# Kernel optimization log

Measured on AMD Instinct MI355X. Metric: run time of the kernel, lower is better.

The kernel has to match this reference:

```python
import jax, jax.numpy as jnp
import numpy as np

SCALE = 1.0 / 4.0      # alpha / dim
MULTIPLIER = 1.0

def _act(h):
    return jax.nn.gelu(h, approximate=False)  # torch nn.GELU(approximate='none')

def setup_inputs() -> dict:
    key = jax.random.key(0)
    ks = jax.random.split(key, 9)
    B, T, D = 64, 77, 768
    N, R = 1024, 4
    return {
        "x":     jax.random.normal(ks[0], (B, T, D), jnp.float32),
        "W_org": jax.random.normal(ks[1], (D, D), jnp.float32) * 0.02,
        "b_org": jax.random.normal(ks[2], (D,), jnp.float32) * 0.02,
        "w1":    jax.random.normal(ks[3], (N, D, R), jnp.float32) * 0.02,
        "b1":    jax.random.normal(ks[4], (N, R), jnp.float32) * 0.02,
        "mid_w": jax.random.normal(ks[5], (N, R, R), jnp.float32) * 0.02,
        "mid_b": jax.random.normal(ks[6], (N, R), jnp.float32) * 0.02,
        "w_out": jax.random.normal(ks[7], (N, R, D), jnp.float32) * 0.02,
        "b_out": jax.random.normal(ks[8], (N, D), jnp.float32) * 0.02,
    }

def reference(x, W_org, b_org, w1, b1, mid_w, mid_b, w_out, b_out):
    # per-concept low-rank MLP: h in [B, T, N, R]
    h = jnp.einsum('btd,ndh->btnh', x, w1) + b1[None, None]
    h = _act(h)
    # repeated 'h' in 'nhh' takes the diagonal of mid_w (elementwise scale),
    # exactly matching torch.einsum semantics in the source.
    h = jnp.einsum('btnh,nhh->btnh', h, mid_w) + mid_b[None, None]
    h = _act(h)
    # fuse out-projection with sum over concepts: sum_n (h_n @ w_out_n) + sum_n b_out_n
    up = jnp.einsum('btnh,nhd->btd', h, w_out) + jnp.sum(b_out, axis=0)
    org = x @ W_org.T + b_org
    return org + up * (MULTIPLIER * SCALE)
```

## Files before the change

kernel.cpp:

```cpp
#include <hip/hip_runtime.h>
#include <hip/hip_bf16.h>

#define M_TOK 4928
#define M_PAD 5120
#define D_DIM 768
#define NR    4096
#define K_CAT 4864
#define KT_ALL 152

typedef __bf16 bf16;
typedef unsigned char u8;
typedef __attribute__((ext_vector_type(8))) __bf16 bf16x8;
typedef __attribute__((ext_vector_type(4))) float f32x4;
typedef __attribute__((address_space(1))) uint32_t gu32;
typedef __attribute__((address_space(3))) uint32_t su32;

#define GLDS(P, LDSP) \
  __builtin_amdgcn_global_load_lds((gu32*)(P), (su32*)(LDSP), 16, 0, 0)

__device__ __forceinline__ uint32_t pk_fp8x4(float a, float b, float c, float d) {
  uint32_t w = 0;
  w = (uint32_t)__builtin_amdgcn_cvt_pk_fp8_f32(a, b, (int)w, false);
  w = (uint32_t)__builtin_amdgcn_cvt_pk_fp8_f32(c, d, (int)w, true);
  return w;
}

__device__ __forceinline__ float act_fast(float v) {
  float e = __builtin_amdgcn_exp2f(v * -2.4554677f);
  return v * __builtin_amdgcn_rcpf(1.0f + e);
}

__device__ __forceinline__ int xcd_swizzle(int orig, int nwg) {
  const int q = nwg >> 3, r = nwg & 7;
  const int x = orig & 7, rest = orig >> 3;
  return (x < r ? x * (q + 1) : r * (q + 1) + (x - r) * q) + rest;
}


__global__ __launch_bounds__(256) void k_prep_x(const float* __restrict__ x,
                                                bf16* __restrict__ Xb) {
  int idx = (blockIdx.x * 256 + threadIdx.x) * 4;
  if (idx >= M_PAD * D_DIM) return;
  int m = idx / D_DIM;
  union { uint2 u; bf16 h[4]; } o;
  if (m < M_TOK) {
    float4 v = *(const float4*)(x + idx);
    o.h[0] = (bf16)v.x; o.h[1] = (bf16)v.y; o.h[2] = (bf16)v.z; o.h[3] = (bf16)v.w;
  } else {
    o.h[0] = o.h[1] = o.h[2] = o.h[3] = (bf16)0.0f;
  }
  *(uint2*)(Xb + idx) = o.u;
}

__global__ __launch_bounds__(256) void k_prep_xq(const float* __restrict__ x,
                                                 u8* __restrict__ Xq) {
  int idx = (blockIdx.x * 256 + threadIdx.x) * 4;
  if (idx >= M_PAD * D_DIM) return;
  int m = idx / D_DIM;
  uint32_t w = 0;
  if (m < M_TOK) {
    float4 v = *(const float4*)(x + idx);
    w = pk_fp8x4(v.x, v.y, v.z, v.w);
  }
  *(uint32_t*)(Xq + idx) = w;
}

__global__ __launch_bounds__(256) void k_prep_w1q(const float* __restrict__ w1,
                                                  u8* __restrict__ W1q) {
  int gid = blockIdx.x * 256 + threadIdx.x;
  int n = gid / 96, oct = gid % 96;
  const float4* src = (const float4*)w1 + (size_t)n * D_DIM + oct * 8;
  float e[4][8];
#pragma unroll
  for (int d = 0; d < 8; ++d) {
    float4 v = src[d];
    e[0][d] = v.x * 64.0f; e[1][d] = v.y * 64.0f;
    e[2][d] = v.z * 64.0f; e[3][d] = v.w * 64.0f;
  }
  size_t base = (size_t)n * 4 * D_DIM + oct * 8;
#pragma unroll
  for (int r = 0; r < 4; ++r) {
    uint2 o;
    o.x = pk_fp8x4(e[r][0], e[r][1], e[r][2], e[r][3]);
    o.y = pk_fp8x4(e[r][4], e[r][5], e[r][6], e[r][7]);
    *(uint2*)(W1q + base + (size_t)r * D_DIM) = o;
  }
}

__global__ __launch_bounds__(256) void k_prep_w2t_t(const float* __restrict__ w_out,
                                                    bf16* __restrict__ W2t) {
  __shared__ float S[64 * 65];
  const int bk = blockIdx.x & 63, bd = blockIdx.x >> 6;
  const int k0 = bk * 64, d0 = bd * 64;
  const int tr = threadIdx.x >> 4;
  const int tc = (threadIdx.x & 15) * 4;
#pragma unroll
  for (int p = 0; p < 4; ++p) {
    const int kr = tr + p * 16;
    float4 v = *(const float4*)(w_out + (size_t)(k0 + kr) * D_DIM + d0 + tc);
    S[kr * 65 + tc + 0] = v.x; S[kr * 65 + tc + 1] = v.y;
    S[kr * 65 + tc + 2] = v.z; S[kr * 65 + tc + 3] = v.w;
  }
  __syncthreads();
#pragma unroll
  for (int p = 0; p < 4; ++p) {
    const int dr = tr + p * 16;
    union { uint2 u; bf16 h[4]; } o;
#pragma unroll
    for (int i = 0; i < 4; ++i) o.h[i] = (bf16)(0.25f * S[(tc + i) * 65 + dr]);
    *(uint2*)(W2t + (size_t)(d0 + dr) * K_CAT + k0 + tc) = o.u;
  }
}

__global__ __launch_bounds__(256) void k_prep_w2t_org(const float* __restrict__ W_org,
                                                      bf16* __restrict__ W2t) {
  int idx = (blockIdx.x * 256 + threadIdx.x) * 4;
  if (idx >= D_DIM * D_DIM) return;
  int d = idx / D_DIM, c = idx % D_DIM;
  float4 v = *(const float4*)(W_org + idx);
  union { uint2 u; bf16 h[4]; } o;
  o.h[0] = (bf16)v.x; o.h[1] = (bf16)v.y; o.h[2] = (bf16)v.z; o.h[3] = (bf16)v.w;
  *(uint2*)(W2t + (size_t)d * K_CAT + NR + c) = o.u;
}

__global__ __launch_bounds__(256) void k_bias_partial(const float* __restrict__ b_out,
                                                      float* __restrict__ partial) {
  int b = blockIdx.x;
  for (int d = threadIdx.x; d < D_DIM; d += 256) {
    float s = 0.0f;
    for (int n = b * 32; n < b * 32 + 32; ++n) s += b_out[n * D_DIM + d];
    partial[b * D_DIM + d] = s;
  }
}

__global__ __launch_bounds__(256) void k_bias_final2(const float* __restrict__ partial,
                                                     const float* __restrict__ b_org,
                                                     const float* __restrict__ mid_w,
                                                     float* __restrict__ bias_total,
                                                     float* __restrict__ diag) {
  int b = blockIdx.x;
  if (b < 3) {
    int d = b * 256 + threadIdx.x;
    if (d >= D_DIM) return;
    float s = 0.0f;
#pragma unroll
    for (int p = 0; p < 32; ++p) s += partial[p * D_DIM + d];
    bias_total[d] = b_org[d] + 0.25f * s;
  } else {
    int j = (b - 3) * 256 + threadIdx.x;
    diag[j] = mid_w[(j >> 2) * 16 + (j & 3) * 5];
  }
}


__device__ __forceinline__ int swz_slot(int kg, int lr) {
  return (kg ^ ((lr >> 1) & 3)) << 3;
}

__device__ __forceinline__ void stage_unit8(const bf16* g, int ld, int row0, int col0,
                                            bf16* lds) {
  const int lane = threadIdx.x & 63;
  const int wave = threadIdx.x >> 6;
  const int src_slot = (lane & 3) ^ ((lane >> 3) & 3);
#pragma unroll
  for (int c = 0; c < 2; ++c) {
    const int chunk = wave * 2 + c;
    const int row = row0 + chunk * 16 + (lane >> 2);
    const bf16* gp = g + (size_t)row * ld + col0 + (src_slot << 3);
    GLDS(gp, lds + chunk * 512);
  }
}


#define G1F_IT(S_, DO_STG, LAST_)                                               \
  {                                                                             \
    if (LAST_) { asm volatile("s_waitcnt vmcnt(0)" ::: "memory"); }             \
    else       { asm volatile("s_waitcnt vmcnt(4)" ::: "memory"); }             \
    asm volatile("s_barrier" ::: "memory");                                     \
    long a0[4], a1[4], b0[4], b1[4];                                            \
    _Pragma("unroll") for (int i = 0; i < 4; ++i) {                             \
      a0[i] = *(const long*)(&As[S_][aOff + i * 1024]);                         \
      a1[i] = *(const long*)(&As[S_][(aOff ^ 32) + i * 1024]);                  \
    }                                                                           \
    _Pragma("unroll") for (int j = 0; j < 4; ++j) {                             \
      b0[j] = *(const long*)(&Bs[S_][bOff + j * 1024]);                         \
      b1[j] = *(const long*)(&Bs[S_][(bOff ^ 32) + j * 1024]);                  \
    }                                                                           \
    if (DO_STG) {                                                               \
      GLDS(aP0, &As[((S_) + 2) % 3][ldsC0]);                                    \
      GLDS(aP1, &As[((S_) + 2) % 3][ldsC1]);                                    \
      GLDS(bP0, &Bs[((S_) + 2) % 3][ldsC0]);                                    \
      GLDS(bP1, &Bs[((S_) + 2) % 3][ldsC1]);                                    \
      aP0 += 64; aP1 += 64; bP0 += 64; bP1 += 64;                               \
    }                                                                           \
    _Pragma("unroll") for (int i = 0; i < 4; ++i)                               \
      _Pragma("unroll") for (int j = 0; j < 4; ++j)                             \
        acc[i][j] = __builtin_amdgcn_mfma_f32_16x16x32_fp8_fp8(b0[j], a0[i], acc[i][j], 0, 0, 0); \
    _Pragma("unroll") for (int i = 0; i < 4; ++i)                               \
      _Pragma("unroll") for (int j = 0; j < 4; ++j)                             \
        acc[i][j] = __builtin_amdgcn_mfma_f32_16x16x32_fp8_fp8(b1[j], a1[i], acc[i][j], 0, 0, 0); \
  }

__global__ __launch_bounds__(256) void k_gemm1(const u8* __restrict__ Xq,
                                               const u8* __restrict__ W1q,
                                               bf16* __restrict__ H2,
                                               const float* __restrict__ b1,
                                               const float* __restrict__ diag,
                                               const float* __restrict__ midb) {
  __shared__ u8 As[3][128 * 64];
  __shared__ u8 Bs[3][128 * 64];
  const int wgid = xcd_swizzle(blockIdx.x, 39 * 32);
  const int bmt = wgid >> 5;
  const int bnt = wgid & 31;
  const int m0 = bmt * 128, n0 = bnt * 128;
  const int lane = threadIdx.x & 63;
  const int wave = threadIdx.x >> 6;
  const int wm = wave >> 1, wn = wave & 1;
  const int lr = lane & 15, kg = lane >> 4;
  const int slotB = (((kg >> 1) ^ ((lr >> 1) & 3)) << 4) + ((kg & 1) << 3);
  const int aOff = (wm * 64 + lr) * 64 + slotB;
  const int bOff = (wn * 64 + lr) * 64 + slotB;

  const int src_slot = (lane & 3) ^ ((lane >> 3) & 3);
  const int srow = (wave * 2) * 16 + (lane >> 2);
  const u8* aP0 = Xq  + (size_t)(m0 + srow) * D_DIM + (src_slot << 4);
  const u8* aP1 = aP0 + 16 * D_DIM;
  const u8* bP0 = W1q + (size_t)(n0 + srow) * D_DIM + (src_slot << 4);
  const u8* bP1 = bP0 + 16 * D_DIM;
  const int ldsC0 = (wave * 2) * 1024, ldsC1 = ldsC0 + 1024;

  f32x4 acc[4][4];
#pragma unroll
  for (int i = 0; i < 4; ++i)
#pragma unroll
    for (int j = 0; j < 4; ++j) acc[i][j] = (f32x4)(0.0f);

  GLDS(aP0, &As[0][ldsC0]); GLDS(aP1, &As[0][ldsC1]);
  GLDS(bP0, &Bs[0][ldsC0]); GLDS(bP1, &Bs[0][ldsC1]);
  aP0 += 64; aP1 += 64; bP0 += 64; bP1 += 64;
  GLDS(aP0, &As[1][ldsC0]); GLDS(aP1, &As[1][ldsC1]);
  GLDS(bP0, &Bs[1][ldsC0]); GLDS(bP1, &Bs[1][ldsC1]);
  aP0 += 64; aP1 += 64; bP0 += 64; bP1 += 64;

  for (int g = 0; g < 3; ++g) {
    G1F_IT(0, true, false)
    G1F_IT(1, true, false)
    G1F_IT(2, true, false)
  }
  G1F_IT(0, true, false)
  G1F_IT(1, false, false)
  G1F_IT(2, false, true)

#pragma unroll
  for (int j = 0; j < 4; ++j) {
    const int jcb = n0 + wn * 64 + j * 16 + kg * 4;
    const float4 b1v = *(const float4*)(b1 + jcb);
    const float4 dgv = *(const float4*)(diag + jcb);
    const float4 mbv = *(const float4*)(midb + jcb);
#pragma unroll
    for (int i = 0; i < 4; ++i) {
      const int mr = m0 + wm * 64 + i * 16 + lr;
      union { uint2 u; bf16 h[4]; } o;
      float h;
      h = act_fast(fmaf(acc[i][j][0], 0.015625f, b1v.x)); o.h[0] = (bf16)act_fast(h * dgv.x + mbv.x);
      h = act_fast(fmaf(acc[i][j][1], 0.015625f, b1v.y)); o.h[1] = (bf16)act_fast(h * dgv.y + mbv.y);
      h = act_fast(fmaf(acc[i][j][2], 0.015625f, b1v.z)); o.h[2] = (bf16)act_fast(h * dgv.z + mbv.z);
      h = act_fast(fmaf(acc[i][j][3], 0.015625f, b1v.w)); o.h[3] = (bf16)act_fast(h * dgv.w + mbv.w);
      *(uint2*)(H2 + (size_t)mr * NR + jcb) = o.u;
    }
  }
}


#define ENGINE(KT0, KT1, STAGE_A, STAGE_B)                                      \
  {                                                                             \
    STAGE_A((KT0) + 0, 0); STAGE_B((KT0) + 0, 0);                               \
    STAGE_A((KT0) + 1, 1); STAGE_B((KT0) + 1, 1);                               \
    STAGE_A((KT0) + 2, 2); STAGE_B((KT0) + 2, 2);                               \
    asm volatile("s_waitcnt vmcnt(8)" ::: "memory");                            \
    asm volatile("s_barrier" ::: "memory");                                     \
    for (int t = (KT0); t < (KT1); ++t) {                                       \
      const int s  = (t - (KT0)) & 3;                                           \
      const int st = (t - (KT0) + 3) & 3;                                       \
      const bool more = (t + 3 < (KT1));                                        \
      bf16x8 a[8], b[4];                                                        \
      _Pragma("unroll") for (int i = 0; i < 4; ++i)                             \
        a[i] = *(const bf16x8*)(As[s] + aBase + i * 512);                       \
      _Pragma("unroll") for (int j = 0; j < 4; ++j)                             \
        b[j] = *(const bf16x8*)(Bs[s] + bBase + j * 512);                       \
      if (more) { STAGE_A(t + 3, st); }                                         \
      asm volatile("s_barrier" ::: "memory");                                   \
      __builtin_amdgcn_s_setprio(1);                                            \
      _Pragma("unroll") for (int i = 0; i < 4; ++i)                             \
        _Pragma("unroll") for (int j = 0; j < 4; ++j)                           \
          acc[i][j] = __builtin_amdgcn_mfma_f32_16x16x32_bf16(b[j], a[i], acc[i][j], 0, 0, 0); \
      __builtin_amdgcn_s_setprio(0);                                            \
      asm volatile("s_barrier" ::: "memory");                                   \
      _Pragma("unroll") for (int i = 0; i < 4; ++i)                             \
        a[4 + i] = *(const bf16x8*)(As[s] + aBase + 2048 + i * 512);            \
      if (more) { STAGE_B(t + 3, st); }                                         \
      {                                                                         \
        int ahead = ((KT1) - 1) - (t + 1);                                      \
        if (ahead >= 2)      { asm volatile("s_waitcnt vmcnt(8)" ::: "memory"); } \
        else if (ahead == 1) { asm volatile("s_waitcnt vmcnt(4)" ::: "memory"); } \
        else                 { asm volatile("s_waitcnt vmcnt(0)" ::: "memory"); } \
      }                                                                         \
      asm volatile("s_barrier" ::: "memory");                                   \
      __builtin_amdgcn_s_setprio(1);                                            \
      _Pragma("unroll") for (int i = 0; i < 4; ++i)                             \
        _Pragma("unroll") for (int j = 0; j < 4; ++j)                           \
          acc[4 + i][j] = __builtin_amdgcn_mfma_f32_16x16x32_bf16(b[j], a[4 + i], acc[4 + i][j], 0, 0, 0); \
      __builtin_amdgcn_s_setprio(0);                                            \
      asm volatile("s_barrier" ::: "memory");                                   \
    }                                                                           \
  }

template <int SPLITS>
__global__ __launch_bounds__(512) void k_gemm2(const bf16* __restrict__ H2,
                                               const bf16* __restrict__ Xb,
                                               const bf16* __restrict__ W2t,
                                               void* __restrict__ outp,
                                               const float* __restrict__ bias) {
  __shared__ bf16 As[4][8192];
  __shared__ bf16 Bs[4][8192];
  const int nwg = 20 * 3 * SPLITS;
  const int wgid = xcd_swizzle(blockIdx.x, nwg);
  const int bmt = wgid / (3 * SPLITS);
  const int rem = wgid % (3 * SPLITS);
  const int ks  = rem / 3;
  const int bnt = rem % 3;
  const int m0 = bmt * 256, n0 = bnt * 256;
  const int lane = threadIdx.x & 63;
  const int wave = threadIdx.x >> 6;
  const int wm = wave >> 2, wn = wave & 3;
  const int lr = lane & 15, kg = lane >> 4;
  const int slotE = swz_slot(kg, lr);
  const int aBase = (wm * 128 + lr) * 32 + slotE;
  const int bBase = (wn * 64 + lr) * 32 + slotE;
  constexpr int KT_PER = KT_ALL / SPLITS;
  const int kt0 = ks * KT_PER, kt1 = kt0 + KT_PER;

  f32x4 acc[8][4];
#pragma unroll
  for (int i = 0; i < 8; ++i)
#pragma unroll
    for (int j = 0; j < 4; ++j) acc[i][j] = (f32x4)(0.0f);

#define G2_SA(kt, buf)                                                  \
  {                                                                     \
    const int k0s = (kt) * 32;                                          \
    if (k0s < NR) stage_unit8(H2, NR, m0, k0s, As[(buf)]);              \
    else          stage_unit8(Xb, D_DIM, m0, k0s - NR, As[(buf)]);      \
  }
#define G2_SB(kt, buf) stage_unit8(W2t, K_CAT, n0, (kt) * 32, Bs[(buf)])
  ENGINE(kt0, kt1, G2_SA, G2_SB)
#undef G2_SA
#undef G2_SB

  if (SPLITS > 1) {
    bf16* dst = (bf16*)outp + (size_t)ks * M_TOK * D_DIM;
#pragma unroll
    for (int j = 0; j < 4; ++j) {
      const int cb = n0 + wn * 64 + j * 16 + kg * 4;
#pragma unroll
      for (int i = 0; i < 8; ++i) {
        const int mr = m0 + wm * 128 + i * 16 + lr;
        if (mr < M_TOK) {
          union { uint2 u; bf16 h[4]; } o;
          o.h[0] = (bf16)acc[i][j][0]; o.h[1] = (bf16)acc[i][j][1];
          o.h[2] = (bf16)acc[i][j][2]; o.h[3] = (bf16)acc[i][j][3];
          *(uint2*)(dst + (size_t)mr * D_DIM + cb) = o.u;
        }
      }
    }
  } else {
    float* dst = (float*)outp;
#pragma unroll
    for (int j = 0; j < 4; ++j) {
      const int cb = n0 + wn * 64 + j * 16 + kg * 4;
      const f32x4 bv = *(const f32x4*)(bias + cb);
#pragma unroll
      for (int i = 0; i < 8; ++i) {
        const int mr = m0 + wm * 128 + i * 16 + lr;
        if (mr < M_TOK) {
          f32x4 o = acc[i][j] + bv;
          *(f32x4*)(dst + (size_t)mr * D_DIM + cb) = o;
        }
      }
    }
  }
}

template <int SPLITS>
__global__ __launch_bounds__(256) void k_reduce(const bf16* __restrict__ padd,
                                                const float* __restrict__ bias,
                                                float* __restrict__ out) {
  int idx = (blockIdx.x * 256 + threadIdx.x) * 4;
  if (idx >= M_TOK * D_DIM) return;
  float4 s = *(const float4*)(bias + (idx % D_DIM));
#pragma unroll
  for (int p = 0; p < SPLITS; ++p) {
    union { uint2 u; bf16 h[4]; } v;
    v.u = *(const uint2*)(padd + (size_t)p * M_TOK * D_DIM + idx);
    s.x += (float)v.h[0]; s.y += (float)v.h[1];
    s.z += (float)v.h[2]; s.w += (float)v.h[3];
  }
  *(float4*)(out + idx) = s;
}


extern "C" void kernel_launch(void* const* d_in, const int* in_sizes, int n_in,
                              void* d_out, int out_size, void* d_ws, size_t ws_size,
                              hipStream_t stream) {
  const float* x     = (const float*)d_in[0];
  const float* W_org = (const float*)d_in[1];
  const float* b_org = (const float*)d_in[2];
  const float* w1    = (const float*)d_in[3];
  const float* b1    = (const float*)d_in[4];
  const float* mid_w = (const float*)d_in[5];
  const float* mid_b = (const float*)d_in[6];
  const float* w_out = (const float*)d_in[7];
  const float* b_out = (const float*)d_in[8];
  float* out = (float*)d_out;

  bf16* Xb   = (bf16*)d_ws;
  bf16* W2t  = Xb  + (size_t)M_PAD * D_DIM;
  bf16* H2   = W2t + (size_t)D_DIM * K_CAT;
  float* bias    = (float*)(H2 + (size_t)M_PAD * NR);
  float* partial = bias + 1024;
  float* diag    = partial + 32 * D_DIM;
  u8*   Xq   = (u8*)(diag + NR);
  u8*   W1q  = Xq + (size_t)M_PAD * D_DIM;
  bf16* padd = (bf16*)(W1q + (size_t)NR * D_DIM);

  const size_t base_bytes = (size_t)((char*)padd - (char*)d_ws);
  const size_t per_split  = (size_t)M_TOK * D_DIM * sizeof(bf16);
  int S = 1;
  if (ws_size >= base_bytes + 4 * per_split)      S = 4;
  else if (ws_size >= base_bytes + 2 * per_split) S = 2;

  k_prep_x      <<<(M_PAD * D_DIM / 4) / 256, 256, 0, stream>>>(x, Xb);
  k_prep_xq     <<<(M_PAD * D_DIM / 4) / 256, 256, 0, stream>>>(x, Xq);
  k_prep_w1q    <<<384, 256, 0, stream>>>(w1, W1q);
  k_prep_w2t_t  <<<64 * 12, 256, 0, stream>>>(w_out, W2t);
  k_prep_w2t_org<<<(D_DIM * D_DIM / 4 + 255) / 256, 256, 0, stream>>>(W_org, W2t);
  k_bias_partial<<<32, 256, 0, stream>>>(b_out, partial);
  k_bias_final2 <<<19, 256, 0, stream>>>(partial, b_org, mid_w, bias, diag);

  k_gemm1<<<39 * 32, 256, 0, stream>>>(Xq, W1q, H2, b1, diag, mid_b);

  const int red_grid = (M_TOK * D_DIM / 4 + 255) / 256;
  if (S == 4) {
    k_gemm2<4><<<20 * 3 * 4, 512, 0, stream>>>(H2, Xb, W2t, padd, bias);
    k_reduce<4><<<red_grid, 256, 0, stream>>>(padd, bias, out);
  } else if (S == 2) {
    k_gemm2<2><<<20 * 3 * 2, 512, 0, stream>>>(H2, Xb, W2t, padd, bias);
    k_reduce<2><<<red_grid, 256, 0, stream>>>(padd, bias, out);
  } else {
    k_gemm2<1><<<20 * 3, 512, 0, stream>>>(H2, Xb, W2t, out, bias);
  }
}
```

Before: 118.9 us.

## Quantize second GEMM to FP8 and split the low-rank and W_org GEMMs

The intermediate activations H2 and the w_out weights are now stored as scaled FP8 instead of bf16. The low-rank out-projection runs as its own fp8 MFMA GEMM with a 4-way K split, using 128x128 tiles and the same pipeline macro as gemm1. The x@W_org part moves to a separate bf16 GEMM that writes bias plus result into out, and the reduce pass then adds the split partials on top. This halves the bytes for the dominant K=4096 operand and doubles MFMA throughput, at the cost of FP8 accuracy loss and an extra kernel launch. The reduce now depends on gemm2b having written out first.

```diff
diff --git a/kernel.cpp b/kernel.cpp
--- a/kernel.cpp
+++ b/kernel.cpp
@@ -3,10 +3,9 @@
 
 #define M_TOK 4928
 #define M_PAD 5120
+#define M_GMM 4992
 #define D_DIM 768
 #define NR    4096
-#define K_CAT 4864
-#define KT_ALL 152
 
 typedef __bf16 bf16;
 typedef unsigned char u8;
@@ -87,8 +86,8 @@
   }
 }
 
-__global__ __launch_bounds__(256) void k_prep_w2t_t(const float* __restrict__ w_out,
-                                                    bf16* __restrict__ W2t) {
+__global__ __launch_bounds__(256) void k_prep_w2q(const float* __restrict__ w_out,
+                                                  u8* __restrict__ W2q) {
   __shared__ float S[64 * 65];
   const int bk = blockIdx.x & 63, bd = blockIdx.x >> 6;
   const int k0 = bk * 64, d0 = bd * 64;
@@ -105,22 +104,20 @@
 #pragma unroll
   for (int p = 0; p < 4; ++p) {
     const int dr = tr + p * 16;
-    union { uint2 u; bf16 h[4]; } o;
-#pragma unroll
-    for (int i = 0; i < 4; ++i) o.h[i] = (bf16)(0.25f * S[(tc + i) * 65 + dr]);
-    *(uint2*)(W2t + (size_t)(d0 + dr) * K_CAT + k0 + tc) = o.u;
-  }
-}
-
-__global__ __launch_bounds__(256) void k_prep_w2t_org(const float* __restrict__ W_org,
-                                                      bf16* __restrict__ W2t) {
+    uint32_t w = pk_fp8x4(16.0f * S[(tc + 0) * 65 + dr], 16.0f * S[(tc + 1) * 65 + dr],
+                          16.0f * S[(tc + 2) * 65 + dr], 16.0f * S[(tc + 3) * 65 + dr]);
+    *(uint32_t*)(W2q + (size_t)(d0 + dr) * NR + k0 + tc) = w;
+  }
+}
+
+__global__ __launch_bounds__(256) void k_prep_worg(const float* __restrict__ W_org,
+                                                   bf16* __restrict__ WorgB) {
   int idx = (blockIdx.x * 256 + threadIdx.x) * 4;
   if (idx >= D_DIM * D_DIM) return;
-  int d = idx / D_DIM, c = idx % D_DIM;
   float4 v = *(const float4*)(W_org + idx);
   union { uint2 u; bf16 h[4]; } o;
   o.h[0] = (bf16)v.x; o.h[1] = (bf16)v.y; o.h[2] = (bf16)v.z; o.h[3] = (bf16)v.w;
-  *(uint2*)(W2t + (size_t)d * K_CAT + NR + c) = o.u;
+  *(uint2*)(WorgB + idx) = o.u;
 }
 
 __global__ __launch_bounds__(256) void k_bias_partial(const float* __restrict__ b_out,
@@ -149,25 +146,6 @@
   } else {
     int j = (b - 3) * 256 + threadIdx.x;
     diag[j] = mid_w[(j >> 2) * 16 + (j & 3) * 5];
-  }
-}
-
-
-__device__ __forceinline__ int swz_slot(int kg, int lr) {
-  return (kg ^ ((lr >> 1) & 3)) << 3;
-}
-
-__device__ __forceinline__ void stage_unit8(const bf16* g, int ld, int row0, int col0,
-                                            bf16* lds) {
-  const int lane = threadIdx.x & 63;
-  const int wave = threadIdx.x >> 6;
-  const int src_slot = (lane & 3) ^ ((lane >> 3) & 3);
-#pragma unroll
-  for (int c = 0; c < 2; ++c) {
-    const int chunk = wave * 2 + c;
-    const int row = row0 + chunk * 16 + (lane >> 2);
-    const bf16* gp = g + (size_t)row * ld + col0 + (src_slot << 3);
-    GLDS(gp, lds + chunk * 512);
   }
 }
 
@@ -203,7 +181,7 @@
 
 __global__ __launch_bounds__(256) void k_gemm1(const u8* __restrict__ Xq,
                                                const u8* __restrict__ W1q,
-                                               bf16* __restrict__ H2,
+                                               u8* __restrict__ H2q,
                                                const float* __restrict__ b1,
                                                const float* __restrict__ diag,
                                                const float* __restrict__ midb) {
@@ -260,146 +238,180 @@
 #pragma unroll
     for (int i = 0; i < 4; ++i) {
       const int mr = m0 + wm * 64 + i * 16 + lr;
-      union { uint2 u; bf16 h[4]; } o;
-      float h;
-      h = act_fast(fmaf(acc[i][j][0], 0.015625f, b1v.x)); o.h[0] = (bf16)act_fast(h * dgv.x + mbv.x);
-      h = act_fast(fmaf(acc[i][j][1], 0.015625f, b1v.y)); o.h[1] = (bf16)act_fast(h * dgv.y + mbv.y);
-      h = act_fast(fmaf(acc[i][j][2], 0.015625f, b1v.z)); o.h[2] = (bf16)act_fast(h * dgv.z + mbv.z);
-      h = act_fast(fmaf(acc[i][j][3], 0.015625f, b1v.w)); o.h[3] = (bf16)act_fast(h * dgv.w + mbv.w);
-      *(uint2*)(H2 + (size_t)mr * NR + jcb) = o.u;
+      float h, f0, f1, f2, f3;
+      h = act_fast(fmaf(acc[i][j][0], 0.015625f, b1v.x)); f0 = act_fast(h * dgv.x + mbv.x);
+      h = act_fast(fmaf(acc[i][j][1], 0.015625f, b1v.y)); f1 = act_fast(h * dgv.y + mbv.y);
+      h = act_fast(fmaf(acc[i][j][2], 0.015625f, b1v.z)); f2 = act_fast(h * dgv.z + mbv.z);
+      h = act_fast(fmaf(acc[i][j][3], 0.015625f, b1v.w)); f3 = act_fast(h * dgv.w + mbv.w);
+      uint32_t w = pk_fp8x4(f0 * 128.0f, f1 * 128.0f, f2 * 128.0f, f3 * 128.0f);
+      *(uint32_t*)(H2q + (size_t)mr * NR + jcb) = w;
     }
   }
 }
 
-
-#define ENGINE(KT0, KT1, STAGE_A, STAGE_B)                                      \
-  {                                                                             \
-    STAGE_A((KT0) + 0, 0); STAGE_B((KT0) + 0, 0);                               \
-    STAGE_A((KT0) + 1, 1); STAGE_B((KT0) + 1, 1);                               \
-    STAGE_A((KT0) + 2, 2); STAGE_B((KT0) + 2, 2);                               \
-    asm volatile("s_waitcnt vmcnt(8)" ::: "memory");                            \
-    asm volatile("s_barrier" ::: "memory");                                     \
-    for (int t = (KT0); t < (KT1); ++t) {                                       \
-      const int s  = (t - (KT0)) & 3;                                           \
-      const int st = (t - (KT0) + 3) & 3;                                       \
-      const bool more = (t + 3 < (KT1));                                        \
-      bf16x8 a[8], b[4];                                                        \
-      _Pragma("unroll") for (int i = 0; i < 4; ++i)                             \
-        a[i] = *(const bf16x8*)(As[s] + aBase + i * 512);                       \
-      _Pragma("unroll") for (int j = 0; j < 4; ++j)                             \
-        b[j] = *(const bf16x8*)(Bs[s] + bBase + j * 512);                       \
-      if (more) { STAGE_A(t + 3, st); }                                         \
-      asm volatile("s_barrier" ::: "memory");                                   \
-      __builtin_amdgcn_s_setprio(1);                                            \
-      _Pragma("unroll") for (int i = 0; i < 4; ++i)                             \
-        _Pragma("unroll") for (int j = 0; j < 4; ++j)                           \
-          acc[i][j] = __builtin_amdgcn_mfma_f32_16x16x32_bf16(b[j], a[i], acc[i][j], 0, 0, 0); \
-      __builtin_amdgcn_s_setprio(0);                                            \
-      asm volatile("s_barrier" ::: "memory");                                   \
-      _Pragma("unroll") for (int i = 0; i < 4; ++i)                             \
-        a[4 + i] = *(const bf16x8*)(As[s] + aBase + 2048 + i * 512);            \
-      if (more) { STAGE_B(t + 3, st); }                                         \
-      {                                                                         \
-        int ahead = ((KT1) - 1) - (t + 1);                                      \
-        if (ahead >= 2)      { asm volatile("s_waitcnt vmcnt(8)" ::: "memory"); } \
-        else if (ahead == 1) { asm volatile("s_waitcnt vmcnt(4)" ::: "memory"); } \
-        else                 { asm volatile("s_waitcnt vmcnt(0)" ::: "memory"); } \
-      }                                                                         \
-      asm volatile("s_barrier" ::: "memory");                                   \
-      __builtin_amdgcn_s_setprio(1);                                            \
-      _Pragma("unroll") for (int i = 0; i < 4; ++i)                             \
-        _Pragma("unroll") for (int j = 0; j < 4; ++j)                           \
-          acc[4 + i][j] = __builtin_amdgcn_mfma_f32_16x16x32_bf16(b[j], a[4 + i], acc[4 + i][j], 0, 0, 0); \
-      __builtin_amdgcn_s_setprio(0);                                            \
-      asm volatile("s_barrier" ::: "memory");                                   \
-    }                                                                           \
-  }
-
-template <int SPLITS>
-__global__ __launch_bounds__(512) void k_gemm2(const bf16* __restrict__ H2,
-                                               const bf16* __restrict__ Xb,
-                                               const bf16* __restrict__ W2t,
-                                               void* __restrict__ outp,
-                                               const float* __restrict__ bias) {
-  __shared__ bf16 As[4][8192];
-  __shared__ bf16 Bs[4][8192];
-  const int nwg = 20 * 3 * SPLITS;
-  const int wgid = xcd_swizzle(blockIdx.x, nwg);
-  const int bmt = wgid / (3 * SPLITS);
-  const int rem = wgid % (3 * SPLITS);
-  const int ks  = rem / 3;
-  const int bnt = rem % 3;
-  const int m0 = bmt * 256, n0 = bnt * 256;
+__global__ __launch_bounds__(256) void k_gemm2a(const u8* __restrict__ H2q,
+                                                const u8* __restrict__ W2q,
+                                                bf16* __restrict__ padd) {
+  __shared__ u8 As[3][128 * 64];
+  __shared__ u8 Bs[3][128 * 64];
+  const int wgid = xcd_swizzle(blockIdx.x, 39 * 6 * 4);
+  const int bmt = wgid / 24;
+  const int rem = wgid % 24;
+  const int ks  = rem / 6;
+  const int bnt = rem % 6;
+  const int m0 = bmt * 128, n0 = bnt * 128;
+  const int kbase = ks * 1024;
   const int lane = threadIdx.x & 63;
   const int wave = threadIdx.x >> 6;
-  const int wm = wave >> 2, wn = wave & 3;
+  const int wm = wave >> 1, wn = wave & 1;
   const int lr = lane & 15, kg = lane >> 4;
-  const int slotE = swz_slot(kg, lr);
-  const int aBase = (wm * 128 + lr) * 32 + slotE;
-  const int bBase = (wn * 64 + lr) * 32 + slotE;
-  constexpr int KT_PER = KT_ALL / SPLITS;
-  const int kt0 = ks * KT_PER, kt1 = kt0 + KT_PER;
-
-  f32x4 acc[8][4];
-#pragma unroll
-  for (int i = 0; i < 8; ++i)
+  const int slotB = (((kg >> 1) ^ ((lr >> 1) & 3)) << 4) + ((kg & 1) << 3);
+  const int aOff = (wm * 64 + lr) * 64 + slotB;
+  const int bOff = (wn * 64 + lr) * 64 + slotB;
+
+  const int src_slot = (lane & 3) ^ ((lane >> 3) & 3);
+  const int srow = (wave * 2) * 16 + (lane >> 2);
+  const u8* aP0 = H2q + (size_t)(m0 + srow) * NR + kbase + (src_slot << 4);
+  const u8* aP1 = aP0 + 16 * NR;
+  const u8* bP0 = W2q + (size_t)(n0 + srow) * NR + kbase + (src_slot << 4);
+  const u8* bP1 = bP0 + 16 * NR;
+  const int ldsC0 = (wave * 2) * 1024, ldsC1 = ldsC0 + 1024;
+
+  f32x4 acc[4][4];
+#pragma unroll
+  for (int i = 0; i < 4; ++i)
 #pragma unroll
     for (int j = 0; j < 4; ++j) acc[i][j] = (f32x4)(0.0f);
 
-#define G2_SA(kt, buf)                                                  \
-  {                                                                     \
-    const int k0s = (kt) * 32;                                          \
-    if (k0s < NR) stage_unit8(H2, NR, m0, k0s, As[(buf)]);              \
-    else          stage_unit8(Xb, D_DIM, m0, k0s - NR, As[(buf)]);      \
-  }
-#define G2_SB(kt, buf) stage_unit8(W2t, K_CAT, n0, (kt) * 32, Bs[(buf)])
-  ENGINE(kt0, kt1, G2_SA, G2_SB)
-#undef G2_SA
-#undef G2_SB
-
-  if (SPLITS > 1) {
-    bf16* dst = (bf16*)outp + (size_t)ks * M_TOK * D_DIM;
-#pragma unroll
-    for (int j = 0; j < 4; ++j) {
-      const int cb = n0 + wn * 64 + j * 16 + kg * 4;
-#pragma unroll
-      for (int i = 0; i < 8; ++i) {
-        const int mr = m0 + wm * 128 + i * 16 + lr;
-        if (mr < M_TOK) {
-          union { uint2 u; bf16 h[4]; } o;
-          o.h[0] = (bf16)acc[i][j][0]; o.h[1] = (bf16)acc[i][j][1];
-          o.h[2] = (bf16)acc[i][j][2]; o.h[3] = (bf16)acc[i][j][3];
-          *(uint2*)(dst + (size_t)mr * D_DIM + cb) = o.u;
-        }
+  GLDS(aP0, &As[0][ldsC0]); GLDS(aP1, &As[0][ldsC1]);
+  GLDS(bP0, &Bs[0][ldsC0]); GLDS(bP1, &Bs[0][ldsC1]);
+  aP0 += 64; aP1 += 64; bP0 += 64; bP1 += 64;
+  GLDS(aP0, &As[1][ldsC0]); GLDS(aP1, &As[1][ldsC1]);
+  GLDS(bP0, &Bs[1][ldsC0]); GLDS(bP1, &Bs[1][ldsC1]);
+  aP0 += 64; aP1 += 64; bP0 += 64; bP1 += 64;
+
+  for (int g = 0; g < 4; ++g) {
+    G1F_IT(0, true, false)
+    G1F_IT(1, true, false)
+    G1F_IT(2, true, false)
+  }
+  G1F_IT(0, true, false)
+  G1F_IT(1, true, false)
+  G1F_IT(2, false, false)
+  G1F_IT(0, false, true)
+
+  bf16* dst = padd + (size_t)ks * M_TOK * D_DIM;
+#pragma unroll
+  for (int j = 0; j < 4; ++j) {
+    const int cb = n0 + wn * 64 + j * 16 + kg * 4;
+#pragma unroll
+    for (int i = 0; i < 4; ++i) {
+      const int mr = m0 + wm * 64 + i * 16 + lr;
+      if (mr < M_TOK) {
+        union { uint2 u; bf16 h[4]; } o;
+        o.h[0] = (bf16)(acc[i][j][0] * 4.8828125e-4f);
+        o.h[1] = (bf16)(acc[i][j][1] * 4.8828125e-4f);
+        o.h[2] = (bf16)(acc[i][j][2] * 4.8828125e-4f);
+        o.h[3] = (bf16)(acc[i][j][3] * 4.8828125e-4f);
+        *(uint2*)(dst + (size_t)mr * D_DIM + cb) = o.u;
       }
     }
-  } else {
-    float* dst = (float*)outp;
-#pragma unroll
-    for (int j = 0; j < 4; ++j) {
-      const int cb = n0 + wn * 64 + j * 16 + kg * 4;
-      const f32x4 bv = *(const f32x4*)(bias + cb);
-#pragma unroll
-      for (int i = 0; i < 8; ++i) {
-        const int mr = m0 + wm * 128 + i * 16 + lr;
-        if (mr < M_TOK) {
-          f32x4 o = acc[i][j] + bv;
-          *(f32x4*)(dst + (size_t)mr * D_DIM + cb) = o;
-        }
+  }
+}
+
+
+#define G1B_IT(S_, DO_STG, LAST_)                                               \
+  {                                                                             \
+    if (LAST_) { asm volatile("s_waitcnt vmcnt(0)" ::: "memory"); }             \
+    else       { asm volatile("s_waitcnt vmcnt(4)" ::: "memory"); }             \
+    asm volatile("s_barrier" ::: "memory");                                     \
+    bf16x8 a_[4], b_[4];                                                        \
+    _Pragma("unroll") for (int i = 0; i < 4; ++i)                               \
+      a_[i] = *(const bf16x8*)(&As[S_][aOff + i * 512]);                        \
+    _Pragma("unroll") for (int j = 0; j < 4; ++j)                               \
+      b_[j] = *(const bf16x8*)(&Bs[S_][bOff + j * 512]);                        \
+    if (DO_STG) {                                                               \
+      GLDS(aP0, &As[((S_) + 2) % 3][ldsC0]);                                    \
+      GLDS(aP1, &As[((S_) + 2) % 3][ldsC1]);                                    \
+      GLDS(bP0, &Bs[((S_) + 2) % 3][ldsC0]);                                    \
+      GLDS(bP1, &Bs[((S_) + 2) % 3][ldsC1]);                                    \
+      aP0 += 32; aP1 += 32; bP0 += 32; bP1 += 32;                               \
+    }                                                                           \
+    _Pragma("unroll") for (int i = 0; i < 4; ++i)                               \
+      _Pragma("unroll") for (int j = 0; j < 4; ++j)                             \
+        acc[i][j] = __builtin_amdgcn_mfma_f32_16x16x32_bf16(b_[j], a_[i], acc[i][j], 0, 0, 0); \
+  }
+
+__global__ __launch_bounds__(256) void k_gemm2b(const bf16* __restrict__ Xb,
+                                                const bf16* __restrict__ WorgB,
+                                                float* __restrict__ out,
+                                                const float* __restrict__ bias) {
+  __shared__ bf16 As[3][128 * 32];
+  __shared__ bf16 Bs[3][128 * 32];
+  const int wgid = xcd_swizzle(blockIdx.x, 39 * 6);
+  const int bmt = wgid / 6;
+  const int bnt = wgid % 6;
+  const int m0 = bmt * 128, n0 = bnt * 128;
+  const int lane = threadIdx.x & 63;
+  const int wave = threadIdx.x >> 6;
+  const int wm = wave >> 1, wn = wave & 1;
+  const int lr = lane & 15, kg = lane >> 4;
+  const int slot = (kg ^ ((lr >> 1) & 3)) << 3;
+  const int aOff = (wm * 64 + lr) * 32 + slot;
+  const int bOff = (wn * 64 + lr) * 32 + slot;
+
+  const int src_slot = (lane & 3) ^ ((lane >> 3) & 3);
+  const int srow = (wave * 2) * 16 + (lane >> 2);
+  const bf16* aP0 = Xb    + (size_t)(m0 + srow) * D_DIM + (src_slot << 3);
+  const bf16* aP1 = aP0 + 16 * D_DIM;
+  const bf16* bP0 = WorgB + (size_t)(n0 + srow) * D_DIM + (src_slot << 3);
+  const bf16* bP1 = bP0 + 16 * D_DIM;
+  const int ldsC0 = (wave * 2) * 512, ldsC1 = ldsC0 + 512;
+
+  f32x4 acc[4][4];
+#pragma unroll
+  for (int i = 0; i < 4; ++i)
+#pragma unroll
+    for (int j = 0; j < 4; ++j) acc[i][j] = (f32x4)(0.0f);
+
+  GLDS(aP0, &As[0][ldsC0]); GLDS(aP1, &As[0][ldsC1]);
+  GLDS(bP0, &Bs[0][ldsC0]); GLDS(bP1, &Bs[0][ldsC1]);
+  aP0 += 32; aP1 += 32; bP0 += 32; bP1 += 32;
+  GLDS(aP0, &As[1][ldsC0]); GLDS(aP1, &As[1][ldsC1]);
+  GLDS(bP0, &Bs[1][ldsC0]); GLDS(bP1, &Bs[1][ldsC1]);
+  aP0 += 32; aP1 += 32; bP0 += 32; bP1 += 32;
+
+  for (int g = 0; g < 7; ++g) {
+    G1B_IT(0, true, false)
+    G1B_IT(1, true, false)
+    G1B_IT(2, true, false)
+  }
+  G1B_IT(0, true, false)
+  G1B_IT(1, false, false)
+  G1B_IT(2, false, true)
+
+#pragma unroll
+  for (int j = 0; j < 4; ++j) {
+    const int cb = n0 + wn * 64 + j * 16 + kg * 4;
+    const f32x4 bv = *(const f32x4*)(bias + cb);
+#pragma unroll
+    for (int i = 0; i < 4; ++i) {
+      const int mr = m0 + wm * 64 + i * 16 + lr;
+      if (mr < M_TOK) {
+        f32x4 o = acc[i][j] + bv;
+        *(f32x4*)(out + (size_t)mr * D_DIM + cb) = o;
       }
     }
   }
 }
 
-template <int SPLITS>
 __global__ __launch_bounds__(256) void k_reduce(const bf16* __restrict__ padd,
-                                                const float* __restrict__ bias,
                                                 float* __restrict__ out) {
   int idx = (blockIdx.x * 256 + threadIdx.x) * 4;
   if (idx >= M_TOK * D_DIM) return;
-  float4 s = *(const float4*)(bias + (idx % D_DIM));
-#pragma unroll
-  for (int p = 0; p < SPLITS; ++p) {
+  float4 s = *(const float4*)(out + idx);
+#pragma unroll
+  for (int p = 0; p < 4; ++p) {
     union { uint2 u; bf16 h[4]; } v;
     v.u = *(const uint2*)(padd + (size_t)p * M_TOK * D_DIM + idx);
     s.x += (float)v.h[0]; s.y += (float)v.h[1];
@@ -423,40 +435,28 @@
   const float* b_out = (const float*)d_in[8];
   float* out = (float*)d_out;
 
-  bf16* Xb   = (bf16*)d_ws;
-  bf16* W2t  = Xb  + (size_t)M_PAD * D_DIM;
-  bf16* H2   = W2t + (size_t)D_DIM * K_CAT;
-  float* bias    = (float*)(H2 + (size_t)M_PAD * NR);
+  bf16* Xb    = (bf16*)d_ws;
+  bf16* WorgB = Xb + (size_t)M_PAD * D_DIM;
+  float* bias    = (float*)(WorgB + (size_t)D_DIM * D_DIM);
   float* partial = bias + 1024;
   float* diag    = partial + 32 * D_DIM;
-  u8*   Xq   = (u8*)(diag + NR);
-  u8*   W1q  = Xq + (size_t)M_PAD * D_DIM;
-  bf16* padd = (bf16*)(W1q + (size_t)NR * D_DIM);
-
-  const size_t base_bytes = (size_t)((char*)padd - (char*)d_ws);
-  const size_t per_split  = (size_t)M_TOK * D_DIM * sizeof(bf16);
-  int S = 1;
-  if (ws_size >= base_bytes + 4 * per_split)      S = 4;
-  else if (ws_size >= base_bytes + 2 * per_split) S = 2;
+  u8* Xq   = (u8*)(diag + NR);
+  u8* W1q  = Xq  + (size_t)M_PAD * D_DIM;
+  u8* W2q  = W1q + (size_t)NR * D_DIM;
+  u8* H2q  = W2q + (size_t)D_DIM * NR;
+  bf16* padd = (bf16*)(H2q + (size_t)M_GMM * NR);
 
   k_prep_x      <<<(M_PAD * D_DIM / 4) / 256, 256, 0, stream>>>(x, Xb);
   k_prep_xq     <<<(M_PAD * D_DIM / 4) / 256, 256, 0, stream>>>(x, Xq);
   k_prep_w1q    <<<384, 256, 0, stream>>>(w1, W1q);
-  k_prep_w2t_t  <<<64 * 12, 256, 0, stream>>>(w_out, W2t);
-  k_prep_w2t_org<<<(D_DIM * D_DIM / 4 + 255) / 256, 256, 0, stream>>>(W_org, W2t);
+  k_prep_w2q    <<<64 * 12, 256, 0, stream>>>(w_out, W2q);
+  k_prep_worg   <<<(D_DIM * D_DIM / 4 + 255) / 256, 256, 0, stream>>>(W_org, WorgB);
   k_bias_partial<<<32, 256, 0, stream>>>(b_out, partial);
   k_bias_final2 <<<19, 256, 0, stream>>>(partial, b_org, mid_w, bias, diag);
 
-  k_gemm1<<<39 * 32, 256, 0, stream>>>(Xq, W1q, H2, b1, diag, mid_b);
-
-  const int red_grid = (M_TOK * D_DIM / 4 + 255) / 256;
-  if (S == 4) {
-    k_gemm2<4><<<20 * 3 * 4, 512, 0, stream>>>(H2, Xb, W2t, padd, bias);
-    k_reduce<4><<<red_grid, 256, 0, stream>>>(padd, bias, out);
-  } else if (S == 2) {
-    k_gemm2<2><<<20 * 3 * 2, 512, 0, stream>>>(H2, Xb, W2t, padd, bias);
-    k_reduce<2><<<red_grid, 256, 0, stream>>>(padd, bias, out);
-  } else {
-    k_gemm2<1><<<20 * 3, 512, 0, stream>>>(H2, Xb, W2t, out, bias);
-  }
-}
+  k_gemm1 <<<39 * 32, 256, 0, stream>>>(Xq, W1q, H2q, b1, diag, mid_b);
+  k_gemm2a<<<39 * 6 * 4, 256, 0, stream>>>(H2q, W2q, padd);
+  k_gemm2b<<<39 * 6, 256, 0, stream>>>(Xb, WorgB, out, bias);
+
+  k_reduce<<<(M_TOK * D_DIM / 4) / 256, 256, 0, stream>>>(padd, out);
+}
```

Result: no change. 121.0 us (+1.8%).
